# Kernel tuning notes

Measured on AMD Instinct MI355X. Metric: run time of the kernel, lower is better.

The kernel has to match this reference:

```python
import jax, jax.numpy as jnp
import numpy as np

SCALE = 20.0
EPS = 1e-8  # torch F.cosine_similarity eps

def _l2norm(x):
    n = jnp.sqrt(jnp.sum(x * x, axis=-1, keepdims=True))
    return x / jnp.maximum(n, EPS)

def setup_inputs() -> dict:
    key = jax.random.key(0)
    k1, k2, k3 = jax.random.split(key, 3)
    B, D, N = 4096, 1024, 4096
    return {
        "query_embeddings": jax.random.normal(k1, (B, D), dtype=jnp.float32),
        "positive_embeddings": jax.random.normal(k2, (B, D), dtype=jnp.float32),
        "negative_embeddings": jax.random.normal(k3, (N, D), dtype=jnp.float32),
    }

def reference(query_embeddings, positive_embeddings, negative_embeddings):
    B = query_embeddings.shape[0]
    q = _l2norm(query_embeddings)                      # (B, D)
    docs = jnp.concatenate([positive_embeddings, negative_embeddings], axis=0)
    d = _l2norm(docs)                                  # (B+N, D)
    scores = SCALE * jnp.einsum("bd,cd->bc", q, d)     # (B, B+N)
    labels = jnp.arange(B)
    logp = jax.nn.log_softmax(scores, axis=-1)
    loss = -jnp.mean(jnp.take_along_axis(logp, labels[:, None], axis=1))
    return loss
```

## Files before the change

### kernel.cpp

```cpp
#include <hip/hip_runtime.h>
#include <stdint.h>

typedef __attribute__((ext_vector_type(8))) short s16x8;
typedef __attribute__((ext_vector_type(4))) float f32x4;

#define DIM 1024
#define NQ 4096
#define NDOC 8192
#define NKT 16

__device__ __forceinline__ unsigned f2bf(float f) {
    unsigned int u = __builtin_bit_cast(unsigned int, f);
    u += 0x7FFFu + ((u >> 16) & 1u);
    return u >> 16;
}

__global__ __launch_bounds__(256) void normalize_kernel(
    const float* __restrict__ q, const float* __restrict__ pos,
    const float* __restrict__ neg, unsigned short* __restrict__ qn,
    unsigned short* __restrict__ dn, float* __restrict__ rowsum) {
    int row = blockIdx.x * 4 + (threadIdx.x >> 6);
    int lane = threadIdx.x & 63;
    const float* src;
    unsigned short* dst;
    if (row < 4096) {
        src = q + (size_t)row * DIM; dst = qn + (size_t)row * DIM;
        if (lane == 0) rowsum[row] = 0.f;
    } else if (row < 8192) {
        src = pos + (size_t)(row - 4096) * DIM; dst = dn + (size_t)(row - 4096) * DIM;
    } else {
        src = neg + (size_t)(row - 8192) * DIM; dst = dn + (size_t)(row - 4096) * DIM;
    }
    float4 v[4];
    float ss = 0.f;
#pragma unroll
    for (int it = 0; it < 4; ++it) {
        v[it] = reinterpret_cast<const float4*>(src)[it * 64 + lane];
        ss += v[it].x * v[it].x + v[it].y * v[it].y + v[it].z * v[it].z + v[it].w * v[it].w;
    }
#pragma unroll
    for (int off = 32; off > 0; off >>= 1) ss += __shfl_xor(ss, off, 64);
    float inv = rsqrtf(ss);
#pragma unroll
    for (int it = 0; it < 4; ++it) {
        uint2 o;
        o.x = f2bf(v[it].x * inv) | (f2bf(v[it].y * inv) << 16);
        o.y = f2bf(v[it].z * inv) | (f2bf(v[it].w * inv) << 16);
        reinterpret_cast<uint2*>(dst)[it * 64 + lane] = o;
    }
}

#define GLOAD_LDS(g, l) __builtin_amdgcn_global_load_lds( \
    (const __attribute__((address_space(1))) void*)(g),   \
    (__attribute__((address_space(3))) void*)(l), 16, 0, 0)

#define STG2(bufByte, kt, r) {                                                        \
    GLOAD_LDS(aG + (r) * 131072 + (kt) * 64, ldsc + (bufByte) + ((r) * 1024 + tid) * 16); \
    GLOAD_LDS(bG + (r) * 131072 + (kt) * 64, ldsc + (bufByte) + 32768 + ((r) * 1024 + tid) * 16); \
  }

#define PHASE(CUR, KS, DOSTG, KT1) {                                              \
    s16x8 bF[4], aF[4];                                                           \
    _Pragma("unroll") for (int n = 0; n < 4; ++n)                                 \
        bF[n] = *(const s16x8*)(ldsc + (CUR) + (bB0 ^ ((KS) * 64)) + n * 2048);   \
    _Pragma("unroll") for (int m = 0; m < 4; ++m)                                 \
        aF[m] = *(const s16x8*)(ldsc + (CUR) + (aB0 ^ ((KS) * 64)) + m * 2048);   \
    if (DOSTG) STG2((CUR) ^ 65536, KT1, 1);                                       \
    __builtin_amdgcn_s_barrier();                                                 \
    __builtin_amdgcn_s_setprio(1);                                                \
    _Pragma("unroll") for (int m = 0; m < 4; ++m)                                 \
        _Pragma("unroll") for (int n = 0; n < 4; ++n)                             \
            acc[m][n] = __builtin_amdgcn_mfma_f32_16x16x32_bf16(                  \
                aF[m], bF[n], acc[m][n], 0, 0, 0);                                \
    __builtin_amdgcn_s_setprio(0);                                                \
  }

__global__ __launch_bounds__(1024, 4) void gemm_lse_kernel(
    const unsigned short* __restrict__ qn, const unsigned short* __restrict__ dn,
    float* __restrict__ rowsum, float* __restrict__ diag) {
    extern __shared__ char ldsc[];
    const int tid = threadIdx.x;
    const int lane = tid & 63;
    const int wid = tid >> 6;
    const int wr = wid >> 2;
    const int wc = wid & 3;
    const int lr = lane & 15;
    const int lk = lane >> 4;

    int bid = blockIdx.x;
    int xcd = bid & 7, local = bid >> 3;
    int brow = (xcd >> 2) * 8 + (local >> 3);
    int bcol = (xcd & 3) * 8 + (local & 7);

    const int srow = tid >> 3;
    const int sslot = (tid & 7) ^ (srow & 7);
    const unsigned short* aG = qn + (size_t)(brow * 256 + srow) * DIM + sslot * 8;
    const unsigned short* bG = dn + (size_t)(bcol * 256 + srow) * DIM + sslot * 8;

    const int s0 = lk ^ (lane & 7);
    const int aB0 = (wr * 64 + lr) * 128 + s0 * 16;
    const int bB0 = 32768 + (wc * 64 + lr) * 128 + s0 * 16;

    f32x4 acc[4][4] = {};

    STG2(0, 0, 0); STG2(0, 0, 1);
    STG2(65536, 1, 0);
    asm volatile("s_waitcnt vmcnt(2)" ::: "memory");
    __builtin_amdgcn_s_barrier();

    for (int t = 0; t < NKT; ++t) {
        const int cur = (t & 1) ? 65536 : 0;
        const bool st = t < NKT - 1;
        PHASE(cur, 0, st, t + 1)
        PHASE(cur, 1, false, 0)
        if (t < NKT - 2) {
            __builtin_amdgcn_s_barrier();
            STG2(cur, t + 2, 0);
            asm volatile("s_waitcnt vmcnt(2)" ::: "memory");
            __builtin_amdgcn_s_barrier();
        } else if (t == NKT - 2) {
            __builtin_amdgcn_s_barrier();
            asm volatile("s_waitcnt vmcnt(0)" ::: "memory");
            __builtin_amdgcn_s_barrier();
        }
    }

#pragma unroll
    for (int m = 0; m < 4; ++m) {
#pragma unroll
        for (int j = 0; j < 4; ++j) {
            float r = 0.f;
#pragma unroll
            for (int n = 0; n < 4; ++n) {
                float s = 20.f * acc[m][n][j] - 20.f;
                r += __expf(s);
            }
#pragma unroll
            for (int off = 1; off < 16; off <<= 1) r += __shfl_xor(r, off, 64);
            if (lr == 0) {
                int row = brow * 256 + wr * 64 + m * 16 + lk * 4 + j;
                atomicAdd(&rowsum[row], r);
            }
        }
    }
    if (brow == bcol) {
#pragma unroll
        for (int m = 0; m < 4; ++m)
#pragma unroll
            for (int j = 0; j < 4; ++j) {
                int tr = wr * 64 + m * 16 + lk * 4 + j;
#pragma unroll
                for (int n = 0; n < 4; ++n)
                    if (wc * 64 + n * 16 + lr == tr)
                        diag[brow * 256 + tr] = 20.f * acc[m][n][j];
            }
    }
}

__global__ __launch_bounds__(1024) void finalize_kernel(
    const float* __restrict__ rowsum, const float* __restrict__ diag,
    float* __restrict__ out) {
    int t = threadIdx.x;
    float s = 0.f;
#pragma unroll
    for (int i = 0; i < 4; ++i) {
        int r = t + i * 1024;
        s += (20.f + __logf(rowsum[r])) - diag[r];
    }
#pragma unroll
    for (int off = 32; off > 0; off >>= 1) s += __shfl_xor(s, off, 64);
    __shared__ float wsum[16];
    if ((t & 63) == 0) wsum[t >> 6] = s;
    __syncthreads();
    if (t == 0) {
        float tot = 0.f;
#pragma unroll
        for (int i = 0; i < 16; ++i) tot += wsum[i];
        out[0] = tot * (1.f / 4096.f);
    }
}

extern "C" void kernel_launch(void* const* d_in, const int* in_sizes, int n_in,
                              void* d_out, int out_size, void* d_ws, size_t ws_size,
                              hipStream_t stream) {
    const float* q   = (const float*)d_in[0];
    const float* pos = (const float*)d_in[1];
    const float* neg = (const float*)d_in[2];
    float* out = (float*)d_out;
    char* ws = (char*)d_ws;
    unsigned short* qn = (unsigned short*)ws;
    unsigned short* dn = (unsigned short*)(ws + (size_t)8 * 1024 * 1024);
    float* rowsum = (float*)(ws + (size_t)24 * 1024 * 1024);
    float* diag   = (float*)(ws + (size_t)24 * 1024 * 1024 + 16384);

    static bool attr_set = false;
    if (!attr_set) {
        (void)hipFuncSetAttribute((const void*)gemm_lse_kernel,
                                  hipFuncAttributeMaxDynamicSharedMemorySize, 131072);
        attr_set = true;
    }

    normalize_kernel<<<3072, 256, 0, stream>>>(q, pos, neg, qn, dn, rowsum);
    gemm_lse_kernel<<<512, 1024, 131072, stream>>>(qn, dn, rowsum, diag);
    finalize_kernel<<<1, 1024, 0, stream>>>(rowsum, diag, out);
}
```

Measured before the change: 163.5 us.

## Halve GEMM block to 512 threads with 128x64 warp tiles and ping-pong fragment prefetch

The GEMM block drops from 16 waves to 8, and each wave now computes a 128x64 tile (8x4 MFMA accumulators) instead of 64x64. Staging of the next K-tile is split into four smaller chunks interleaved between MFMA groups. LDS fragment reads for the next sub-step are issued in software-pipelined X/Y/b0/b1 registers ahead of use, and one of the per-iteration barriers is removed. The aim is more MFMA work per LDS read and barrier, plus better overlap of loads with compute. The cost is higher register pressure and fewer waves to hide latency.

Measured after the change: 168.8 us. 1.03x slower.

```diff
diff --git a/kernel.cpp b/kernel.cpp
--- a/kernel.cpp
+++ b/kernel.cpp
@@ -55,27 +55,22 @@
     (__attribute__((address_space(3))) void*)(l), 16, 0, 0)
 
 #define STG2(bufByte, kt, r) {                                                        \
-    GLOAD_LDS(aG + (r) * 131072 + (kt) * 64, ldsc + (bufByte) + ((r) * 1024 + tid) * 16); \
-    GLOAD_LDS(bG + (r) * 131072 + (kt) * 64, ldsc + (bufByte) + 32768 + ((r) * 1024 + tid) * 16); \
+    GLOAD_LDS(aG + (r) * 65536 + (kt) * 64, ldsc + (bufByte) + ((r) * 512 + tid) * 16); \
+    GLOAD_LDS(bG + (r) * 65536 + (kt) * 64, ldsc + (bufByte) + 32768 + ((r) * 512 + tid) * 16); \
   }
 
-#define PHASE(CUR, KS, DOSTG, KT1) {                                              \
-    s16x8 bF[4], aF[4];                                                           \
-    _Pragma("unroll") for (int n = 0; n < 4; ++n)                                 \
-        bF[n] = *(const s16x8*)(ldsc + (CUR) + (bB0 ^ ((KS) * 64)) + n * 2048);   \
-    _Pragma("unroll") for (int m = 0; m < 4; ++m)                                 \
-        aF[m] = *(const s16x8*)(ldsc + (CUR) + (aB0 ^ ((KS) * 64)) + m * 2048);   \
-    if (DOSTG) STG2((CUR) ^ 65536, KT1, 1);                                       \
-    __builtin_amdgcn_s_barrier();                                                 \
-    __builtin_amdgcn_s_setprio(1);                                                \
-    _Pragma("unroll") for (int m = 0; m < 4; ++m)                                 \
-        _Pragma("unroll") for (int n = 0; n < 4; ++n)                             \
-            acc[m][n] = __builtin_amdgcn_mfma_f32_16x16x32_bf16(                  \
-                aF[m], bF[n], acc[m][n], 0, 0, 0);                                \
-    __builtin_amdgcn_s_setprio(0);                                                \
-  }
-
-__global__ __launch_bounds__(1024, 4) void gemm_lse_kernel(
+#define ARD(curB, sl, blk) (*(const s16x8*)(ldsc + (curB) + aRowB + (blk) * 2048 + (sl)))
+#define BRD(curB, sl, n)   (*(const s16x8*)(ldsc + (curB) + bRowB + (n) * 2048 + (sl)))
+
+#define MFMA16(F, B, base)                                                       \
+    __builtin_amdgcn_s_setprio(1);                                               \
+    _Pragma("unroll") for (int m = 0; m < 4; ++m)                                \
+        _Pragma("unroll") for (int n = 0; n < 4; ++n)                            \
+            acc[(base) + m][n] = __builtin_amdgcn_mfma_f32_16x16x32_bf16(        \
+                F[m], B[n], acc[(base) + m][n], 0, 0, 0);                        \
+    __builtin_amdgcn_s_setprio(0);
+
+__global__ __launch_bounds__(512, 2) void gemm_lse_kernel(
     const unsigned short* __restrict__ qn, const unsigned short* __restrict__ dn,
     float* __restrict__ rowsum, float* __restrict__ diag) {
     extern __shared__ char ldsc[];
@@ -97,36 +92,62 @@
     const unsigned short* aG = qn + (size_t)(brow * 256 + srow) * DIM + sslot * 8;
     const unsigned short* bG = dn + (size_t)(bcol * 256 + srow) * DIM + sslot * 8;
 
-    const int s0 = lk ^ (lane & 7);
-    const int aB0 = (wr * 64 + lr) * 128 + s0 * 16;
-    const int bB0 = 32768 + (wc * 64 + lr) * 128 + s0 * 16;
-
-    f32x4 acc[4][4] = {};
-
-    STG2(0, 0, 0); STG2(0, 0, 1);
+    const int sl0 = (lk ^ (lane & 7)) * 16;
+    const int sl1 = ((4 + lk) ^ (lane & 7)) * 16;
+    const int aRowB = (wr * 128 + lr) * 128;
+    const int bRowB = 32768 + (wc * 64 + lr) * 128;
+
+    f32x4 acc[8][4] = {};
+    s16x8 X[4], Y[4], b0[4], b1[4];
+
+#pragma unroll
+    for (int r = 0; r < 4; ++r) STG2(0, 0, r);
     STG2(65536, 1, 0);
     asm volatile("s_waitcnt vmcnt(2)" ::: "memory");
     __builtin_amdgcn_s_barrier();
+#pragma unroll
+    for (int m = 0; m < 4; ++m) X[m] = ARD(0, sl0, m);
+#pragma unroll
+    for (int n = 0; n < 4; ++n) b0[n] = BRD(0, sl0, n);
 
     for (int t = 0; t < NKT; ++t) {
-        const int cur = (t & 1) ? 65536 : 0;
-        const bool st = t < NKT - 1;
-        PHASE(cur, 0, st, t + 1)
-        PHASE(cur, 1, false, 0)
+        const int cur = (t & 1) * 65536;
+        const int nxt = cur ^ 65536;
+        const bool stg = t < NKT - 1;
+#pragma unroll
+        for (int m = 0; m < 4; ++m) Y[m] = ARD(cur, sl0, 4 + m);
+#pragma unroll
+        for (int n = 0; n < 4; ++n) b1[n] = BRD(cur, sl1, n);
+        if (stg) STG2(nxt, t + 1, 1);
+        MFMA16(X, b0, 0)
+#pragma unroll
+        for (int m = 0; m < 4; ++m) X[m] = ARD(cur, sl1, m);
+        if (stg) STG2(nxt, t + 1, 2);
+        MFMA16(Y, b0, 4)
+#pragma unroll
+        for (int m = 0; m < 4; ++m) Y[m] = ARD(cur, sl1, 4 + m);
+        if (stg) STG2(nxt, t + 1, 3);
+        MFMA16(X, b1, 0)
+        asm volatile("s_waitcnt lgkmcnt(0)" ::: "memory");
+        __builtin_amdgcn_s_barrier();
         if (t < NKT - 2) {
-            __builtin_amdgcn_s_barrier();
             STG2(cur, t + 2, 0);
             asm volatile("s_waitcnt vmcnt(2)" ::: "memory");
-            __builtin_amdgcn_s_barrier();
         } else if (t == NKT - 2) {
-            __builtin_amdgcn_s_barrier();
             asm volatile("s_waitcnt vmcnt(0)" ::: "memory");
-            __builtin_amdgcn_s_barrier();
         }
-    }
-
-#pragma unroll
-    for (int m = 0; m < 4; ++m) {
+        __builtin_amdgcn_s_barrier();
+        if (stg) {
+#pragma unroll
+            for (int m = 0; m < 4; ++m) X[m] = ARD(nxt, sl0, m);
+#pragma unroll
+            for (int n = 0; n < 4; ++n) b0[n] = BRD(nxt, sl0, n);
+        }
+        MFMA16(Y, b1, 4)
+    }
+
+#pragma unroll
+    for (int m = 0; m < 8; ++m) {
 #pragma unroll
         for (int j = 0; j < 4; ++j) {
             float r = 0.f;
@@ -138,17 +159,17 @@
 #pragma unroll
             for (int off = 1; off < 16; off <<= 1) r += __shfl_xor(r, off, 64);
             if (lr == 0) {
-                int row = brow * 256 + wr * 64 + m * 16 + lk * 4 + j;
+                int row = brow * 256 + wr * 128 + m * 16 + lk * 4 + j;
                 atomicAdd(&rowsum[row], r);
             }
         }
     }
     if (brow == bcol) {
 #pragma unroll
-        for (int m = 0; m < 4; ++m)
+        for (int m = 0; m < 8; ++m)
 #pragma unroll
             for (int j = 0; j < 4; ++j) {
-                int tr = wr * 64 + m * 16 + lk * 4 + j;
+                int tr = wr * 128 + m * 16 + lk * 4 + j;
 #pragma unroll
                 for (int n = 0; n < 4; ++n)
                     if (wc * 64 + n * 16 + lr == tr)
@@ -201,6 +222,6 @@
     }
 
     normalize_kernel<<<3072, 256, 0, stream>>>(q, pos, neg, qn, dn, rowsum);
-    gemm_lse_kernel<<<512, 1024, 131072, stream>>>(qn, dn, rowsum, diag);
+    gemm_lse_kernel<<<512, 512, 131072, stream>>>(qn, dn, rowsum, diag);
     finalize_kernel<<<1, 1024, 0, stream>>>(rowsum, diag, out);
 }
```
